# Performance work log

Measured on AMD Instinct MI355X. Metric: run time of the kernel, lower is better.

The kernel has to match this reference:

```python
import jax, jax.numpy as jnp
import numpy as np

# MPI 15-joint skeleton: 0 head,1 neck,2 rsho,3 relb,4 rwri,5 lsho,6 lelb,7 lwri,
# 8 rhip,9 rknee,10 rankle,11 lhip,12 lknee,13 lankle,14 hip/spine
LEFT_BONES = np.array([[1, 5], [5, 6], [6, 7], [14, 11], [11, 12], [12, 13]], dtype=np.int32)
RIGHT_BONES = np.array([[1, 2], [2, 3], [3, 4], [14, 8], [8, 9], [9, 10]], dtype=np.int32)

FLEN = 512.0   # focal length (pixels)
CX, CY = 512.0, 256.0  # principal point
R_CAM = np.eye(3, dtype=np.float32)  # fixed drone->camera rotation

B, J = 262144, 15


def setup_inputs() -> dict:
    key = jax.random.key(0)
    k1, k2, k3, k4 = jax.random.split(key, 4)
    pose3d = jax.random.normal(k1, (B, 3, J), dtype=jnp.float32)
    pose_2d = jax.random.normal(k2, (B, 2, J), dtype=jnp.float32)
    # near-identity rotations so camera-frame depth stays well away from 0
    R_drone = jnp.eye(3, dtype=jnp.float32)[None] + 0.05 * jax.random.normal(k3, (B, 3, 3), dtype=jnp.float32)
    C_drone = jax.random.normal(k4, (B, 3, 1), dtype=jnp.float32)
    C_drone = C_drone.at[:, 2, :].add(-5.0)  # put camera behind the pose along z
    return {"pose3d": pose3d, "pose_2d": pose_2d, "R_drone": R_drone, "C_drone": C_drone}


def _forward(pose3d, pose_2d, R_drone, C_drone):
    lb = jnp.asarray(LEFT_BONES)
    rb = jnp.asarray(RIGHT_BONES)
    # bone length (squared) for each side: gather endpoints, diff, sum over xyz
    dl = pose3d[:, :, lb[:, 0]] - pose3d[:, :, lb[:, 1]]   # [B,3,6]
    dr = pose3d[:, :, rb[:, 0]] - pose3d[:, :, rb[:, 1]]   # [B,3,6]
    len_l = jnp.sum(dl * dl, axis=1)                        # [B,6]
    len_r = jnp.sum(dr * dr, axis=1)                        # [B,6]
    sym = jnp.mean((len_l - len_r) ** 2)                    # mean over bones and batch

    # take_bone_projection: camera frame = R_cam @ R_drone^T @ (P - C), pinhole projection
    P = jnp.einsum('bji,bjk->bik', R_drone, pose3d - C_drone)          # R_drone^T @ (P - C), [B,3,J]
    P = jnp.einsum('ij,bjk->bik', jnp.asarray(R_CAM), P)               # [B,3,J]
    z = P[:, 2]                                                         # [B,J]
    u = FLEN * P[:, 0] / z + CX
    v = FLEN * P[:, 1] / z + CY
    projected_2d = jnp.stack([u, v], axis=1)                            # [B,2,J]
    proj = jnp.mean((projected_2d - pose_2d) ** 2)
    return jnp.stack([sym, proj])


def reference(pose3d, pose_2d, R_drone, C_drone):
    return _forward(pose3d, pose_2d, R_drone, C_drone)
```

## Files before the change

kernel.cpp:

```cpp
#include <hip/hip_runtime.h>


__global__ __launch_bounds__(256) void pose_calib_main(
    const float* __restrict__ pose3d,
    const float* __restrict__ pose2d,
    const float* __restrict__ Rd,
    const float* __restrict__ Cd,
    double* __restrict__ partial,
    int B)
{
    const int b = blockIdx.x * blockDim.x + threadIdx.x;
    double sym_d = 0.0, proj_d = 0.0;

    if (b < B) {
        const float* p3 = pose3d + (size_t)b * 45;
        float X[45];
        #pragma unroll
        for (int i = 0; i < 45; ++i) X[i] = p3[i];

        const int lb0[6] = {1,5,6,14,11,12};
        const int lb1[6] = {5,6,7,11,12,13};
        const int rb0[6] = {1,2,3,14,8,9};
        const int rb1[6] = {2,3,4,8,9,10};
        #pragma unroll
        for (int k = 0; k < 6; ++k) {
            double ll = 0.0, lr = 0.0;
            #pragma unroll
            for (int c = 0; c < 3; ++c) {
                double dl = (double)X[c*15 + lb0[k]] - (double)X[c*15 + lb1[k]];
                double dr = (double)X[c*15 + rb0[k]] - (double)X[c*15 + rb1[k]];
                ll += dl * dl;
                lr += dr * dr;
            }
            double d = ll - lr;
            sym_d += d * d;
        }

        const float* Rp = Rd + (size_t)b * 9;
        const float* Cp = Cd + (size_t)b * 3;
        const double R00 = Rp[0], R01 = Rp[1], R02 = Rp[2];
        const double R10 = Rp[3], R11 = Rp[4], R12 = Rp[5];
        const double R20 = Rp[6], R21 = Rp[7], R22 = Rp[8];
        const double C0 = Cp[0], C1 = Cp[1], C2 = Cp[2];

        const float* p2 = pose2d + (size_t)b * 30;
        #pragma unroll
        for (int j = 0; j < 15; ++j) {
            double q0 = (double)X[j]      - C0;
            double q1 = (double)X[15 + j] - C1;
            double q2 = (double)X[30 + j] - C2;
            double P0 = R00*q0 + R10*q1 + R20*q2;
            double P1 = R01*q0 + R11*q1 + R21*q2;
            double P2 = R02*q0 + R12*q1 + R22*q2;
            double rz = 1.0 / P2;
            double u = 512.0 * P0 * rz + 512.0;
            double v = 512.0 * P1 * rz + 256.0;
            double du = u - (double)p2[j];
            double dv = v - (double)p2[15 + j];
            proj_d += du*du + dv*dv;
        }
    }

    #pragma unroll
    for (int off = 32; off > 0; off >>= 1) {
        sym_d  += __shfl_down(sym_d,  off, 64);
        proj_d += __shfl_down(proj_d, off, 64);
    }
    __shared__ double s_sym[4], s_proj[4];
    const int lane = threadIdx.x & 63;
    const int wid  = threadIdx.x >> 6;
    if (lane == 0) { s_sym[wid] = sym_d; s_proj[wid] = proj_d; }
    __syncthreads();
    if (threadIdx.x == 0) {
        partial[2*(size_t)blockIdx.x]     = s_sym[0] + s_sym[1] + s_sym[2] + s_sym[3];
        partial[2*(size_t)blockIdx.x + 1] = s_proj[0] + s_proj[1] + s_proj[2] + s_proj[3];
    }
}

__global__ __launch_bounds__(256) void pose_calib_finish(
    const double* __restrict__ partial, int nblk,
    float* __restrict__ out, double inv_n_sym, double inv_n_proj)
{
    double ss = 0.0, pp = 0.0;
    for (int i = threadIdx.x; i < nblk; i += 256) {
        ss += partial[2*(size_t)i];
        pp += partial[2*(size_t)i + 1];
    }
    #pragma unroll
    for (int off = 32; off > 0; off >>= 1) {
        ss += __shfl_down(ss, off, 64);
        pp += __shfl_down(pp, off, 64);
    }
    __shared__ double s_s[4], s_p[4];
    const int lane = threadIdx.x & 63;
    const int wid  = threadIdx.x >> 6;
    if (lane == 0) { s_s[wid] = ss; s_p[wid] = pp; }
    __syncthreads();
    if (threadIdx.x == 0) {
        double S = s_s[0] + s_s[1] + s_s[2] + s_s[3];
        double P = s_p[0] + s_p[1] + s_p[2] + s_p[3];
        out[0] = (float)(S * inv_n_sym);
        out[1] = (float)(P * inv_n_proj);
    }
}

extern "C" void kernel_launch(void* const* d_in, const int* in_sizes, int n_in,
                              void* d_out, int out_size, void* d_ws, size_t ws_size,
                              hipStream_t stream) {
    const float* pose3d = (const float*)d_in[0];
    const float* pose2d = (const float*)d_in[1];
    const float* Rd     = (const float*)d_in[2];
    const float* Cd     = (const float*)d_in[3];

    const int B = in_sizes[3] / 3;
    const int threads = 256;
    const int nblk = (B + threads - 1) / threads;

    double* partial = (double*)d_ws;

    pose_calib_main<<<nblk, threads, 0, stream>>>(pose3d, pose2d, Rd, Cd, partial, B);
    pose_calib_finish<<<1, threads, 0, stream>>>(
        partial, nblk, (float*)d_out,
        1.0 / ((double)B * 6.0), 1.0 / ((double)B * 30.0));
}
```

Before: 24.58 us.

## Stage per-slab inputs into LDS with global_load_lds for coalesced reads

The main kernel now uses single-wave blocks that each handle four 64-pose slabs. Each slab's pose3d, pose2d, rotation and camera data is copied into LDS with coalesced 16-byte global_load_lds transfers, and threads then read their own strided records from LDS. This replaces the old per-thread strided global loads, which were poorly coalesced. The change also drops the cross-wave shared-memory reduction and reads partials as double2 in the finish kernel. Risks are LDS bank conflicts on the stride-45 reads, lower occupancy from the large LDS footprint, and correctness of the hand-written waitcnt ordering.

```diff
diff --git a/kernel.cpp b/kernel.cpp
--- a/kernel.cpp
+++ b/kernel.cpp
@@ -1,7 +1,19 @@
 #include <hip/hip_runtime.h>
 
 
-__global__ __launch_bounds__(256) void pose_calib_main(
+typedef const __attribute__((address_space(1))) void* gas1_t;
+typedef __attribute__((address_space(3))) void* las3_t;
+
+__device__ __forceinline__ void gl16(const float* g, float* l) {
+    __builtin_amdgcn_global_load_lds((gas1_t)g, (las3_t)l, 16, 0, 0);
+}
+__device__ __forceinline__ void gl4(const float* g, float* l) {
+    __builtin_amdgcn_global_load_lds((gas1_t)g, (las3_t)l, 4, 0, 0);
+}
+
+#define SLABS 4
+
+__global__ __launch_bounds__(64) void pose_calib_main(
     const float* __restrict__ pose3d,
     const float* __restrict__ pose2d,
     const float* __restrict__ Rd,
@@ -9,55 +21,111 @@
     double* __restrict__ partial,
     int B)
 {
-    const int b = blockIdx.x * blockDim.x + threadIdx.x;
+    __shared__ float sX[2880];
+    __shared__ float sP2[1920];
+    __shared__ float sR[576];
+    __shared__ float sC[192];
+
+    const int lane = threadIdx.x;
     double sym_d = 0.0, proj_d = 0.0;
 
-    if (b < B) {
-        const float* p3 = pose3d + (size_t)b * 45;
-        float X[45];
-        #pragma unroll
-        for (int i = 0; i < 45; ++i) X[i] = p3[i];
+    const long long slab0 = (long long)blockIdx.x * SLABS;
 
-        const int lb0[6] = {1,5,6,14,11,12};
-        const int lb1[6] = {5,6,7,11,12,13};
-        const int rb0[6] = {1,2,3,14,8,9};
-        const int rb1[6] = {2,3,4,8,9,10};
-        #pragma unroll
-        for (int k = 0; k < 6; ++k) {
-            double ll = 0.0, lr = 0.0;
+    for (int s = 0; s < SLABS; ++s) {
+        const long long p0 = (slab0 + s) * 64;
+        if (p0 >= (long long)B) break;
+        const bool full = (p0 + 64 <= (long long)B);
+
+        float X[45], pu[15], pv[15], Rr[9], Cc[3];
+        bool active;
+
+        if (full) {
+            if (s > 0)
+                asm volatile("s_waitcnt lgkmcnt(0)" ::: "memory");
+
+            const float* g3 = pose3d + p0 * 45;
+            const float* g2 = pose2d + p0 * 30;
+            const float* gR = Rd + p0 * 9;
+            const float* gC = Cd + p0 * 3;
+
             #pragma unroll
-            for (int c = 0; c < 3; ++c) {
-                double dl = (double)X[c*15 + lb0[k]] - (double)X[c*15 + lb1[k]];
-                double dr = (double)X[c*15 + rb0[k]] - (double)X[c*15 + rb1[k]];
-                ll += dl * dl;
-                lr += dr * dr;
+            for (int k = 0; k < 11; ++k) gl16(g3 + k * 256 + lane * 4, sX + k * 256);
+            gl4(g3 + 2816 + lane, sX + 2816);
+            #pragma unroll
+            for (int k = 0; k < 7; ++k) gl16(g2 + k * 256 + lane * 4, sP2 + k * 256);
+            gl4(g2 + 1792 + lane, sP2 + 1792);
+            gl4(g2 + 1856 + lane, sP2 + 1856);
+            gl16(gR + lane * 4, sR);
+            gl16(gR + 256 + lane * 4, sR + 256);
+            gl4(gR + 512 + lane, sR + 512);
+            gl4(gC + lane, sC);
+            gl4(gC + 64 + lane, sC + 64);
+            gl4(gC + 128 + lane, sC + 128);
+
+            asm volatile("s_waitcnt vmcnt(0)" ::: "memory");
+
+            active = true;
+            #pragma unroll
+            for (int i = 0; i < 45; ++i) X[i] = sX[lane * 45 + i];
+            #pragma unroll
+            for (int j = 0; j < 15; ++j) { pu[j] = sP2[lane * 30 + j]; pv[j] = sP2[lane * 30 + 15 + j]; }
+            #pragma unroll
+            for (int k = 0; k < 9; ++k) Rr[k] = sR[lane * 9 + k];
+            #pragma unroll
+            for (int c = 0; c < 3; ++c) Cc[c] = sC[lane * 3 + c];
+        } else {
+            const long long p = p0 + lane;
+            active = (p < (long long)B);
+            if (active) {
+                const float* g3 = pose3d + p * 45;
+                const float* g2 = pose2d + p * 30;
+                const float* gR = Rd + p * 9;
+                const float* gC = Cd + p * 3;
+                #pragma unroll
+                for (int i = 0; i < 45; ++i) X[i] = g3[i];
+                #pragma unroll
+                for (int j = 0; j < 15; ++j) { pu[j] = g2[j]; pv[j] = g2[15 + j]; }
+                #pragma unroll
+                for (int k = 0; k < 9; ++k) Rr[k] = gR[k];
+                #pragma unroll
+                for (int c = 0; c < 3; ++c) Cc[c] = gC[c];
             }
-            double d = ll - lr;
-            sym_d += d * d;
         }
 
-        const float* Rp = Rd + (size_t)b * 9;
-        const float* Cp = Cd + (size_t)b * 3;
-        const double R00 = Rp[0], R01 = Rp[1], R02 = Rp[2];
-        const double R10 = Rp[3], R11 = Rp[4], R12 = Rp[5];
-        const double R20 = Rp[6], R21 = Rp[7], R22 = Rp[8];
-        const double C0 = Cp[0], C1 = Cp[1], C2 = Cp[2];
+        if (active) {
+            const int lb0[6] = {1, 5, 6, 14, 11, 12}, lb1[6] = {5, 6, 7, 11, 12, 13};
+            const int rb0[6] = {1, 2, 3, 14, 8, 9},   rb1[6] = {2, 3, 4, 8, 9, 10};
+            #pragma unroll
+            for (int k = 0; k < 6; ++k) {
+                double ll = 0.0, lr = 0.0;
+                #pragma unroll
+                for (int c = 0; c < 3; ++c) {
+                    double dl = (double)X[c * 15 + lb0[k]] - (double)X[c * 15 + lb1[k]];
+                    double dr = (double)X[c * 15 + rb0[k]] - (double)X[c * 15 + rb1[k]];
+                    ll += dl * dl;
+                    lr += dr * dr;
+                }
+                double d = ll - lr;
+                sym_d += d * d;
+            }
 
-        const float* p2 = pose2d + (size_t)b * 30;
-        #pragma unroll
-        for (int j = 0; j < 15; ++j) {
-            double q0 = (double)X[j]      - C0;
-            double q1 = (double)X[15 + j] - C1;
-            double q2 = (double)X[30 + j] - C2;
-            double P0 = R00*q0 + R10*q1 + R20*q2;
-            double P1 = R01*q0 + R11*q1 + R21*q2;
-            double P2 = R02*q0 + R12*q1 + R22*q2;
-            double rz = 1.0 / P2;
-            double u = 512.0 * P0 * rz + 512.0;
-            double v = 512.0 * P1 * rz + 256.0;
-            double du = u - (double)p2[j];
-            double dv = v - (double)p2[15 + j];
-            proj_d += du*du + dv*dv;
+            const double R00 = Rr[0], R01 = Rr[1], R02 = Rr[2];
+            const double R10 = Rr[3], R11 = Rr[4], R12 = Rr[5];
+            const double R20 = Rr[6], R21 = Rr[7], R22 = Rr[8];
+            const double C0 = Cc[0], C1 = Cc[1], C2 = Cc[2];
+            #pragma unroll
+            for (int j = 0; j < 15; ++j) {
+                double q0 = (double)X[j]      - C0;
+                double q1 = (double)X[15 + j] - C1;
+                double q2 = (double)X[30 + j] - C2;
+                double P0 = R00 * q0 + R10 * q1 + R20 * q2;
+                double P1 = R01 * q0 + R11 * q1 + R21 * q2;
+                double P2 = R02 * q0 + R12 * q1 + R22 * q2;
+                double rz = 1.0 / P2;
+                double du = 512.0 * P0 * rz + 512.0 - (double)pu[j];
+                double dv = 512.0 * P1 * rz + 256.0 - (double)pv[j];
+                proj_d += du * du + dv * dv;
+            }
         }
     }
 
@@ -66,14 +134,9 @@
         sym_d  += __shfl_down(sym_d,  off, 64);
         proj_d += __shfl_down(proj_d, off, 64);
     }
-    __shared__ double s_sym[4], s_proj[4];
-    const int lane = threadIdx.x & 63;
-    const int wid  = threadIdx.x >> 6;
-    if (lane == 0) { s_sym[wid] = sym_d; s_proj[wid] = proj_d; }
-    __syncthreads();
-    if (threadIdx.x == 0) {
-        partial[2*(size_t)blockIdx.x]     = s_sym[0] + s_sym[1] + s_sym[2] + s_sym[3];
-        partial[2*(size_t)blockIdx.x + 1] = s_proj[0] + s_proj[1] + s_proj[2] + s_proj[3];
+    if (lane == 0) {
+        partial[2 * (size_t)blockIdx.x]     = sym_d;
+        partial[2 * (size_t)blockIdx.x + 1] = proj_d;
     }
 }
 
@@ -81,10 +144,12 @@
     const double* __restrict__ partial, int nblk,
     float* __restrict__ out, double inv_n_sym, double inv_n_proj)
 {
+    const double2* p2 = (const double2*)partial;
     double ss = 0.0, pp = 0.0;
     for (int i = threadIdx.x; i < nblk; i += 256) {
-        ss += partial[2*(size_t)i];
-        pp += partial[2*(size_t)i + 1];
+        double2 v = p2[i];
+        ss += v.x;
+        pp += v.y;
     }
     #pragma unroll
     for (int off = 32; off > 0; off >>= 1) {
@@ -113,13 +178,13 @@
     const float* Cd     = (const float*)d_in[3];
 
     const int B = in_sizes[3] / 3;
-    const int threads = 256;
-    const int nblk = (B + threads - 1) / threads;
+    const int nslab = (B + 63) / 64;
+    const int nblk  = (nslab + SLABS - 1) / SLABS;
 
     double* partial = (double*)d_ws;
 
-    pose_calib_main<<<nblk, threads, 0, stream>>>(pose3d, pose2d, Rd, Cd, partial, B);
-    pose_calib_finish<<<1, threads, 0, stream>>>(
+    pose_calib_main<<<nblk, 64, 0, stream>>>(pose3d, pose2d, Rd, Cd, partial, B);
+    pose_calib_finish<<<1, 256, 0, stream>>>(
         partial, nblk, (float*)d_out,
         1.0 / ((double)B * 6.0), 1.0 / ((double)B * 30.0));
 }
```

Result: slower. 26.66 us (+8.4%).
